# Kernel tuning notes

Hardware: AMD Instinct MI355X
Metric: run time of the kernel (lower is better)

Reference implementation:

```python
import jax, jax.numpy as jnp
import numpy as np

VAR0, VAR1 = 0.1, 0.2          # SSD variances
IOU_THRESH = 0.5
NUM_CLASSES = 21
NEGPOS_RATIO = 3
ALPHA = 1.0


def mid_to_corner(b):
    # [cx,cy,w,h] -> [xmin,ymin,xmax,ymax]
    return jnp.concatenate([b[:, :2] - b[:, 2:] / 2, b[:, :2] + b[:, 2:] / 2], axis=1)


def jaccard(box_a, box_b):
    # box_a [n,4], box_b [P,4] corner form -> IoU [n,P]
    lt = jnp.maximum(box_a[:, None, :2], box_b[None, :, :2])
    rb = jnp.minimum(box_a[:, None, 2:], box_b[None, :, 2:])
    wh = jnp.clip(rb - lt, 0.0)
    inter = wh[..., 0] * wh[..., 1]
    area_a = (box_a[:, 2] - box_a[:, 0]) * (box_a[:, 3] - box_a[:, 1])
    area_b = (box_b[:, 2] - box_b[:, 0]) * (box_b[:, 3] - box_b[:, 1])
    union = area_a[:, None] + area_b[None, :] - inter
    return inter / union


def encode_offset(matched, priors):
    # matched corner form [P,4], priors center form [P,4]
    g_cxcy = ((matched[:, :2] + matched[:, 2:]) / 2 - priors[:, :2]) / (VAR0 * priors[:, 2:])
    g_wh = jnp.log((matched[:, 2:] - matched[:, :2]) / priors[:, 2:]) / VAR1
    return jnp.concatenate([g_cxcy, g_wh], axis=1)


def match_one(gt_box, gt_cls, valid, priors_corner, priors_mid):
    # gt_box [n,4], gt_cls [n], valid [n] bool; priors [P,4]
    n = gt_box.shape[0]
    P = priors_corner.shape[0]
    ovl = jaccard(gt_box, priors_corner)                    # [n,P]
    ovl = jnp.where(valid[:, None], ovl, -1.0)              # mask padded GTs
    best_truth_idx = jnp.argmax(ovl, axis=0)                # [P]
    best_truth_ovl = jnp.max(ovl, axis=0)                   # [P]
    best_prior_idx = jnp.argmax(ovl, axis=1)                # [n]
    bpi = jnp.where(valid, best_prior_idx, P)               # OOB for padded -> dropped
    best_truth_ovl = best_truth_ovl.at[bpi].set(2.0, mode='drop')
    best_truth_idx = best_truth_idx.at[bpi].set(jnp.arange(n), mode='drop')
    matches = gt_box[best_truth_idx]                        # [P,4]
    loc = encode_offset(matches, priors_mid)                # [P,4]
    conf = gt_cls[best_truth_idx].astype(jnp.int32) + 1     # [P]
    conf = jnp.where(best_truth_ovl < IOU_THRESH, 0, conf)
    return loc, conf


def setup_inputs() -> dict:
    key = jax.random.key(0)
    k = jax.random.split(key, 8)
    B, P, C, NMAX = 64, 8732, 21, 50
    confidence = jax.random.normal(k[0], (B, P, C), dtype=jnp.float32)
    location = 0.1 * jax.random.normal(k[1], (B, P, 4), dtype=jnp.float32)
    cxcy = jax.random.uniform(k[2], (P, 2), minval=0.05, maxval=0.95)
    pwh = jax.random.uniform(k[3], (P, 2), minval=0.05, maxval=0.4)
    prior_boxes = jnp.concatenate([cxcy, pwh], axis=1).astype(jnp.float32)
    xymin = jax.random.uniform(k[4], (B, NMAX, 2), minval=0.0, maxval=0.6)
    gwh = jax.random.uniform(k[5], (B, NMAX, 2), minval=0.05, maxval=0.35)
    cls = jax.random.randint(k[6], (B, NMAX), 0, C - 1).astype(jnp.float32)
    labels = jnp.concatenate([xymin, xymin + gwh, cls[..., None]], axis=-1).astype(jnp.float32)
    obj_count = jax.random.randint(k[7], (B, 1), 1, NMAX + 1).astype(jnp.int32)
    return {"confidence": confidence, "location": location,
            "prior_boxes": prior_boxes, "labels": labels, "obj_count": obj_count}


def reference(confidence, location, prior_boxes, labels, obj_count):
    B, P, C = confidence.shape
    NMAX = labels.shape[1]
    priors_corner = mid_to_corner(prior_boxes)
    valid = jnp.arange(NMAX)[None, :] < obj_count            # [B,NMAX]
    loc_t, conf_t = jax.vmap(match_one, in_axes=(0, 0, 0, None, None))(
        labels[..., :4], labels[..., 4], valid, priors_corner, prior_boxes)
    # loc_t [B,P,4] float, conf_t [B,P] int32

    pos = conf_t > 0                                          # [B,P]
    # smooth-L1 over positive anchors (sum reduction)
    d = jnp.abs(location - loc_t)
    sl1 = jnp.where(d < 1.0, 0.5 * d * d, d - 0.5)
    loss_loc = jnp.sum(sl1 * pos[..., None].astype(sl1.dtype))

    # hard negative mining score: global-max logsumexp minus target logit
    bc = confidence.reshape(-1, C)
    x_max = jnp.max(bc)
    lse = jnp.log(jnp.sum(jnp.exp(bc - x_max), axis=1)) + x_max
    tgt_logit = jnp.take_along_axis(bc, conf_t.reshape(-1, 1), axis=1)[:, 0]
    loss_c = (lse - tgt_logit).reshape(B, P)
    loss_c = jnp.where(pos, 0.0, loss_c)
    loss_idx = jnp.argsort(-loss_c, axis=1)                   # descending sort
    idx_rank = jnp.argsort(loss_idx, axis=1)
    num_pos = jnp.sum(pos.astype(jnp.int32), axis=1, keepdims=True)   # [B,1]
    num_neg = jnp.clip(NEGPOS_RATIO * num_pos, None, P - 1)
    neg = idx_rank < num_neg                                  # [B,P]

    # standard cross entropy over selected (pos|neg) anchors, sum reduction
    logp = jax.nn.log_softmax(confidence, axis=-1)            # [B,P,C]
    nll = -jnp.take_along_axis(logp, conf_t[..., None], axis=-1)[..., 0]
    sel = jnp.logical_or(pos, neg)
    loss_conf = jnp.sum(nll * sel.astype(nll.dtype))

    N = jnp.sum(num_pos).astype(confidence.dtype)
    return (ALPHA * loss_loc / N, loss_conf / N)
```

## Files before the change

kernel.cpp:

```cpp
#include <hip/hip_runtime.h>
#include <math.h>

#define Bn 64
#define Pn 8732
#define Cn 21
#define NMAXn 50
#define PX 35
#define Wn 16

template <int C>
__device__ __forceinline__ float dppf(float x) {
    return __int_as_float(__builtin_amdgcn_update_dpp(0, __float_as_int(x), C, 0xf, 0xf, true));
}
template <int C>
__device__ __forceinline__ int dppi(int x) {
    return __builtin_amdgcn_update_dpp(0, x, C, 0xf, 0xf, true);
}
__device__ __forceinline__ float wave_max_f(float x) {
    x = fmaxf(x, dppf<0x111>(x));
    x = fmaxf(x, dppf<0x112>(x));
    x = fmaxf(x, dppf<0x114>(x));
    x = fmaxf(x, dppf<0x118>(x));
    x = fmaxf(x, dppf<0x142>(x));
    x = fmaxf(x, dppf<0x143>(x));
    return x;
}
__device__ __forceinline__ float wave_sum_f(float x) {
    x += dppf<0x111>(x); x += dppf<0x112>(x); x += dppf<0x114>(x);
    x += dppf<0x118>(x); x += dppf<0x142>(x); x += dppf<0x143>(x);
    return x;
}
__device__ __forceinline__ int wave_sum_i(int x) {
    x += dppi<0x111>(x); x += dppi<0x112>(x); x += dppi<0x114>(x);
    x += dppi<0x118>(x); x += dppi<0x142>(x); x += dppi<0x143>(x);
    return x;
}

__global__ __launch_bounds__(256) void k_bpp(const float* __restrict__ labels,
                                             const int* __restrict__ objc,
                                             const float* __restrict__ priors,
                                             int* __restrict__ match,
                                             unsigned long long* __restrict__ bpk) {
    const int b = blockIdx.y;
    const int px = blockIdx.x;
    const int tid = threadIdx.x;
    const int lane = tid & 63, wid = tid >> 6;
    const int cnt = objc[b];
    const float* lb = labels + b * NMAXn * 5;

    const int p = px * 256 + tid;
    const bool valid = p < Pn;
    const int pcl = valid ? p : (Pn - 1);
    const float4 pr = reinterpret_cast<const float4*>(priors)[pcl];
    const float px0 = pr.x - 0.5f * pr.z, py0 = pr.y - 0.5f * pr.w;
    const float px1 = pr.x + 0.5f * pr.z, py1 = pr.y + 0.5f * pr.w;
    const float parea = (px1 - px0) * (py1 - py0);

    float best = -1.0f;
    int bidx = 0;
    for (int n = 0; n < cnt; ++n) {
        const float gx0 = lb[n * 5 + 0], gy0 = lb[n * 5 + 1];
        const float gx1 = lb[n * 5 + 2], gy1 = lb[n * 5 + 3];
        const float lx = fmaxf(gx0, px0), ly = fmaxf(gy0, py0);
        const float rx = fminf(gx1, px1), ry = fminf(gy1, py1);
        const float w = fmaxf(rx - lx, 0.0f), h = fmaxf(ry - ly, 0.0f);
        const float inter = w * h;
        const float ga = (gx1 - gx0) * (gy1 - gy0);
        const float q = inter / (ga + parea - inter);
        if (q > best) { best = q; bidx = n; }
        const float qr = valid ? q : 0.0f;
        const float m = wave_max_f(qr);
        const float s_q = __int_as_float(__builtin_amdgcn_readlane(__float_as_int(m), 63));
        const unsigned long long mask = __ballot(qr == s_q);
        const int first = __ffsll(mask) - 1;
        if (lane == 0) {
            const int pw = px * 256 + (wid << 6) + first;
            const unsigned long long key =
                ((unsigned long long)__float_as_uint(s_q) << 32) |
                (unsigned long long)(65535 - pw);
            bpk[(size_t)(b * NMAXn + n) * (PX * 4) + px * 4 + wid] = key;
        }
    }
    if (valid) match[(size_t)b * Pn + p] = (bidx << 1) | (best >= 0.5f ? 1 : 0);
}

__global__ __launch_bounds__(64) void k_bpr(const int* __restrict__ objc,
                                            const unsigned long long* __restrict__ bpk,
                                            int* __restrict__ match,
                                            int* __restrict__ done) {
    __shared__ int sbp[NMAXn];
    const int b = blockIdx.x;
    const int tid = threadIdx.x;
    if (b == 0 && tid == 0) *done = 0;
    const int cnt = objc[b];
    if (tid < cnt) {
        const size_t g0 = (size_t)(b * NMAXn + tid) * (PX * 4);
        unsigned long long best = 0ull;
        for (int t = 0; t < PX * 4; ++t) {
            const unsigned long long k = bpk[g0 + t];
            best = (k > best) ? k : best;
        }
        sbp[tid] = 65535 - (int)(best & 0xFFFFull);
    }
    __syncthreads();
    if (tid < cnt) {
        const int myp = sbp[tid];
        bool win = true;
        for (int n2 = tid + 1; n2 < cnt; ++n2) win = win && (sbp[n2] != myp);
        if (win) match[(size_t)b * Pn + myp] = (tid << 1) | 1;
    }
}

__global__ __launch_bounds__(256) void k_main(const float* __restrict__ conf,
                                              const float* __restrict__ loc,
                                              const float* __restrict__ priors,
                                              const float* __restrict__ labels,
                                              const int* __restrict__ match,
                                              float* __restrict__ lc,
                                              float* __restrict__ part_loc,
                                              float* __restrict__ part_nll,
                                              int* __restrict__ part_np) {
    const int b = blockIdx.y;
    const int px = blockIdx.x;
    const int p0 = px * 256;
    const int tid = threadIdx.x;
    const int rows = min(256, Pn - p0);
    const int p = p0 + ((tid < rows) ? tid : 0);
    const size_t gi = (size_t)b * Pn + p;
    const int w = match[gi];

    const float* row = conf + gi * Cn;
    float a[Cn];
#pragma unroll
    for (int j = 0; j < Cn; ++j) a[j] = row[j];

    float my_loc = 0.0f, my_nll = 0.0f;
    int my_np = 0;
    if (tid < rows) {
        const int ti = w >> 1;
        int ct = 0;
        if (w & 1) ct = (int)labels[(b * NMAXn + ti) * 5 + 4] + 1;
        float m = a[0];
#pragma unroll
        for (int j = 1; j < Cn; ++j) m = fmaxf(m, a[j]);
        float s2 = 0.0f;
#pragma unroll
        for (int j = 0; j < Cn; ++j) s2 += __expf(a[j] - m);
        float tgt = a[0];
#pragma unroll
        for (int j = 1; j < Cn; ++j) tgt = (ct == j) ? a[j] : tgt;
        const float nll = __logf(s2) + m - tgt;
        if (ct > 0) {
            lc[gi] = 0.0f;
            my_np = 1;
            my_nll = nll;
            const float* lbp = labels + (b * NMAXn + ti) * 5;
            const float gx0 = lbp[0], gy0 = lbp[1], gx1 = lbp[2], gy1 = lbp[3];
            const float4 pr = reinterpret_cast<const float4*>(priors)[p];
            const float tx = ((gx0 + gx1) * 0.5f - pr.x) / (0.1f * pr.z);
            const float ty = ((gy0 + gy1) * 0.5f - pr.y) / (0.1f * pr.w);
            const float tw = __logf((gx1 - gx0) / pr.z) * 5.0f;
            const float th = __logf((gy1 - gy0) / pr.w) * 5.0f;
            const float4 l = reinterpret_cast<const float4*>(loc)[gi];
            float d;
            d = fabsf(l.x - tx); my_loc += (d < 1.0f) ? 0.5f * d * d : d - 0.5f;
            d = fabsf(l.y - ty); my_loc += (d < 1.0f) ? 0.5f * d * d : d - 0.5f;
            d = fabsf(l.z - tw); my_loc += (d < 1.0f) ? 0.5f * d * d : d - 0.5f;
            d = fabsf(l.w - th); my_loc += (d < 1.0f) ? 0.5f * d * d : d - 0.5f;
        } else {
            lc[gi] = nll;
        }
    }
    my_loc = wave_sum_f(my_loc);
    my_nll = wave_sum_f(my_nll);
    my_np = wave_sum_i(my_np);
    __shared__ float rl[4], rn[4];
    __shared__ int rp[4];
    const int wid = tid >> 6, lane = tid & 63;
    if (lane == 63) { rl[wid] = my_loc; rn[wid] = my_nll; rp[wid] = my_np; }
    __syncthreads();
    if (tid == 0) {
        const int g = b * PX + px;
        part_loc[g] = rl[0] + rl[1] + rl[2] + rl[3];
        part_nll[g] = rn[0] + rn[1] + rn[2] + rn[3];
        part_np[g] = rp[0] + rp[1] + rp[2] + rp[3];
    }
}

__global__ __launch_bounds__(1024) void k_neg(const float* __restrict__ lc,
                                              const float* __restrict__ part_loc,
                                              const float* __restrict__ part_nll,
                                              const int* __restrict__ part_np,
                                              float* __restrict__ negsum,
                                              int* __restrict__ done,
                                              float* __restrict__ out) {
    const int b = blockIdx.x;
    const int tid = threadIdx.x;
    const int lane = tid & 63, wid = tid >> 6;
    __shared__ int redc[2][Wn];
    __shared__ float redf[Wn], redf2[Wn];
    __shared__ int redi[Wn];
    __shared__ int np_sh, islast;

    const int NV = Pn / 4;
    const float4* src = reinterpret_cast<const float4*>(lc + (size_t)b * Pn);
    const float4 sent = make_float4(-1.0f, -1.0f, -1.0f, -1.0f);
    float4 r0 = (tid < NV) ? src[tid] : sent;
    float4 r1 = (tid + 1024 < NV) ? src[tid + 1024] : sent;
    float4 r2 = (tid + 2048 < NV) ? src[tid + 2048] : sent;

    if (tid < 64) {
        int npl = (tid < PX) ? part_np[b * PX + tid] : 0;
        npl = wave_sum_i(npl);
        if (tid == 63) np_sh = npl;
    }
    __syncthreads();
    const int k = min(3 * np_sh, Pn - 1);

    unsigned lo = 0u, hi = 0x7F800000u;
#pragma unroll 1
    for (int it = 0; it < 31; ++it) {
        const unsigned mid = lo + ((hi - lo) >> 1);
        const float fm = __uint_as_float(mid);
        int c = (r0.x >= fm) + (r0.y >= fm) + (r0.z >= fm) + (r0.w >= fm)
              + (r1.x >= fm) + (r1.y >= fm) + (r1.z >= fm) + (r1.w >= fm)
              + (r2.x >= fm) + (r2.y >= fm) + (r2.z >= fm) + (r2.w >= fm);
        c = wave_sum_i(c);
        if (lane == 63) redc[it & 1][wid] = c;
        __syncthreads();
        int tot = 0;
#pragma unroll
        for (int w = 0; w < Wn; ++w) tot += redc[it & 1][w];
        if (tot >= k) lo = mid;
        else hi = mid;
    }
    const float v = __uint_as_float(lo);

    float sm = 0.0f;
    int c = 0;
    if (r0.x > v) { sm += r0.x; ++c; }
    if (r0.y > v) { sm += r0.y; ++c; }
    if (r0.z > v) { sm += r0.z; ++c; }
    if (r0.w > v) { sm += r0.w; ++c; }
    if (r1.x > v) { sm += r1.x; ++c; }
    if (r1.y > v) { sm += r1.y; ++c; }
    if (r1.z > v) { sm += r1.z; ++c; }
    if (r1.w > v) { sm += r1.w; ++c; }
    if (r2.x > v) { sm += r2.x; ++c; }
    if (r2.y > v) { sm += r2.y; ++c; }
    if (r2.z > v) { sm += r2.z; ++c; }
    if (r2.w > v) { sm += r2.w; ++c; }
    sm = wave_sum_f(sm);
    c = wave_sum_i(c);
    if (lane == 63) { redf[wid] = sm; redi[wid] = c; }
    __syncthreads();
    if (tid == 0) {
        float st = 0.0f;
        int ct = 0;
#pragma unroll
        for (int w = 0; w < Wn; ++w) { st += redf[w]; ct += redi[w]; }
        negsum[b] = st + (float)(k - ct) * v;
        __threadfence();
        islast = (atomicAdd(done, 1) == Bn - 1) ? 1 : 0;
    }
    __syncthreads();
    if (!islast) return;
    __threadfence();

    float sl = 0.0f, sn = 0.0f;
    int np = 0;
    for (int i = tid; i < Bn * PX; i += 1024) {
        sl += part_loc[i];
        sn += part_nll[i];
        np += part_np[i];
    }
    if (tid < Bn) sn += negsum[tid];
    sl = wave_sum_f(sl);
    sn = wave_sum_f(sn);
    np = wave_sum_i(np);
    if (lane == 63) { redf[wid] = sn; redf2[wid] = sl; redi[wid] = np; }
    __syncthreads();
    if (tid == 0) {
        float tsl = 0.0f, tsn = 0.0f;
        int tnp = 0;
#pragma unroll
        for (int w = 0; w < Wn; ++w) { tsl += redf2[w]; tsn += redf[w]; tnp += redi[w]; }
        const float fN = (float)tnp;
        out[0] = tsl / fN;
        out[1] = tsn / fN;
    }
}

extern "C" void kernel_launch(void* const* d_in, const int* in_sizes, int n_in,
                              void* d_out, int out_size, void* d_ws, size_t ws_size,
                              hipStream_t stream) {
    const float* conf = (const float*)d_in[0];
    const float* loc = (const float*)d_in[1];
    const float* priors = (const float*)d_in[2];
    const float* labels = (const float*)d_in[3];
    const int* objc = (const int*)d_in[4];
    float* out = (float*)d_out;

    unsigned long long* bpk = (unsigned long long*)d_ws;
    float* part_loc = (float*)(bpk + (size_t)Bn * NMAXn * PX * 4);
    float* part_nll = part_loc + Bn * PX;
    int* part_np = (int*)(part_nll + Bn * PX);
    float* negsum = (float*)(part_np + Bn * PX);
    int* match = (int*)(negsum + Bn);
    float* lc = (float*)(match + (size_t)Bn * Pn);
    int* done = (int*)(lc + (size_t)Bn * Pn);

    dim3 g(PX, Bn);
    k_bpp<<<g, 256, 0, stream>>>(labels, objc, priors, match, bpk);
    k_bpr<<<Bn, 64, 0, stream>>>(objc, bpk, match, done);
    k_main<<<g, 256, 0, stream>>>(conf, loc, priors, labels, match, lc,
                                  part_loc, part_nll, part_np);
    k_neg<<<Bn, 1024, 0, stream>>>(lc, part_loc, part_nll, part_np, negsum, done, out);
}
```

Measured before the change: 78.65 us.

## Fuse matching, forced-match fixup and loss pass into one kernel

Merges the three kernels for per-prior matching, best-prior reduction and the per-anchor loss into one kernel. Each block now stages its confidence rows in shared memory, reduces per-GT best-prior keys with a global atomicMax, and the last block of each image computes correction terms for priors forced to a GT. Those corrections are passed to the negative-mining kernel, which zeroes the forced priors' scores. This removes two launches and the round trip of the match array through global memory. In exchange it adds a memset, atomics, a serial per-image fixup in the last block, and recomputation of IoU and loss for forced priors.

Measured after the change: 242.8 us. 3.09x slower.

```diff
diff --git a/kernel.cpp b/kernel.cpp
--- a/kernel.cpp
+++ b/kernel.cpp
@@ -17,12 +17,9 @@
     return __builtin_amdgcn_update_dpp(0, x, C, 0xf, 0xf, true);
 }
 __device__ __forceinline__ float wave_max_f(float x) {
-    x = fmaxf(x, dppf<0x111>(x));
-    x = fmaxf(x, dppf<0x112>(x));
-    x = fmaxf(x, dppf<0x114>(x));
-    x = fmaxf(x, dppf<0x118>(x));
-    x = fmaxf(x, dppf<0x142>(x));
-    x = fmaxf(x, dppf<0x143>(x));
+    x = fmaxf(x, dppf<0x111>(x)); x = fmaxf(x, dppf<0x112>(x));
+    x = fmaxf(x, dppf<0x114>(x)); x = fmaxf(x, dppf<0x118>(x));
+    x = fmaxf(x, dppf<0x142>(x)); x = fmaxf(x, dppf<0x143>(x));
     return x;
 }
 __device__ __forceinline__ float wave_sum_f(float x) {
@@ -36,26 +33,65 @@
     return x;
 }
 
-__global__ __launch_bounds__(256) void k_bpp(const float* __restrict__ labels,
+__device__ __forceinline__ float smoothl1_enc(const float4 l, const float4 pr,
+                                              float gx0, float gy0, float gx1, float gy1) {
+    const float tx = ((gx0 + gx1) * 0.5f - pr.x) / (0.1f * pr.z);
+    const float ty = ((gy0 + gy1) * 0.5f - pr.y) / (0.1f * pr.w);
+    const float tw = __logf((gx1 - gx0) / pr.z) * 5.0f;
+    const float th = __logf((gy1 - gy0) / pr.w) * 5.0f;
+    float s = 0.0f, d;
+    d = fabsf(l.x - tx); s += (d < 1.0f) ? 0.5f * d * d : d - 0.5f;
+    d = fabsf(l.y - ty); s += (d < 1.0f) ? 0.5f * d * d : d - 0.5f;
+    d = fabsf(l.z - tw); s += (d < 1.0f) ? 0.5f * d * d : d - 0.5f;
+    d = fabsf(l.w - th); s += (d < 1.0f) ? 0.5f * d * d : d - 0.5f;
+    return s;
+}
+
+__global__ __launch_bounds__(256) void k_all(const float* __restrict__ conf,
+                                             const float* __restrict__ loc,
+                                             const float* __restrict__ priors,
+                                             const float* __restrict__ labels,
                                              const int* __restrict__ objc,
-                                             const float* __restrict__ priors,
-                                             int* __restrict__ match,
-                                             unsigned long long* __restrict__ bpk) {
+                                             float* __restrict__ lc,
+                                             float* __restrict__ part_loc,
+                                             float* __restrict__ part_nll,
+                                             int* __restrict__ part_np,
+                                             unsigned long long* __restrict__ slot,
+                                             int* __restrict__ done_b,
+                                             int* __restrict__ fix_np,
+                                             float* __restrict__ fix_nll,
+                                             float* __restrict__ fix_loc,
+                                             int* __restrict__ forced_cnt,
+                                             int* __restrict__ flist) {
     const int b = blockIdx.y;
     const int px = blockIdx.x;
+    const int p0 = px * 256;
     const int tid = threadIdx.x;
     const int lane = tid & 63, wid = tid >> 6;
+    const int rows = min(256, Pn - p0);
     const int cnt = objc[b];
     const float* lb = labels + b * NMAXn * 5;
 
-    const int p = px * 256 + tid;
+    __shared__ float sconf[256 * Cn];
+    __shared__ float lab[NMAXn * 5];
+    __shared__ unsigned long long wkey[NMAXn][4];
+    __shared__ float rl[4], rn[4];
+    __shared__ int rp[4];
+    __shared__ int sbp[NMAXn];
+    __shared__ int islast_s;
+
+    const float4* src = reinterpret_cast<const float4*>(conf + ((size_t)b * Pn + p0) * Cn);
+    const int n4 = rows * Cn / 4;
+    for (int i = tid; i < n4; i += 256) reinterpret_cast<float4*>(sconf)[i] = src[i];
+    for (int i = tid; i < NMAXn * 5; i += 256) lab[i] = labels[b * NMAXn * 5 + i];
+
+    const int p = p0 + tid;
     const bool valid = p < Pn;
     const int pcl = valid ? p : (Pn - 1);
     const float4 pr = reinterpret_cast<const float4*>(priors)[pcl];
     const float px0 = pr.x - 0.5f * pr.z, py0 = pr.y - 0.5f * pr.w;
     const float px1 = pr.x + 0.5f * pr.z, py1 = pr.y + 0.5f * pr.w;
     const float parea = (px1 - px0) * (py1 - py0);
-
     float best = -1.0f;
     int bidx = 0;
     for (int n = 0; n < cnt; ++n) {
@@ -69,104 +105,46 @@
         const float q = inter / (ga + parea - inter);
         if (q > best) { best = q; bidx = n; }
         const float qr = valid ? q : 0.0f;
-        const float m = wave_max_f(qr);
-        const float s_q = __int_as_float(__builtin_amdgcn_readlane(__float_as_int(m), 63));
-        const unsigned long long mask = __ballot(qr == s_q);
-        const int first = __ffsll(mask) - 1;
+        const float mx = wave_max_f(qr);
+        const float s_q = __int_as_float(__builtin_amdgcn_readlane(__float_as_int(mx), 63));
+        const unsigned long long bmask = __ballot(qr == s_q);
         if (lane == 0) {
-            const int pw = px * 256 + (wid << 6) + first;
-            const unsigned long long key =
-                ((unsigned long long)__float_as_uint(s_q) << 32) |
-                (unsigned long long)(65535 - pw);
-            bpk[(size_t)(b * NMAXn + n) * (PX * 4) + px * 4 + wid] = key;
-        }
-    }
-    if (valid) match[(size_t)b * Pn + p] = (bidx << 1) | (best >= 0.5f ? 1 : 0);
-}
-
-__global__ __launch_bounds__(64) void k_bpr(const int* __restrict__ objc,
-                                            const unsigned long long* __restrict__ bpk,
-                                            int* __restrict__ match,
-                                            int* __restrict__ done) {
-    __shared__ int sbp[NMAXn];
-    const int b = blockIdx.x;
-    const int tid = threadIdx.x;
-    if (b == 0 && tid == 0) *done = 0;
-    const int cnt = objc[b];
+            const int first = __ffsll(bmask) - 1;
+            const int pw = p0 + (wid << 6) + first;
+            wkey[n][wid] = ((unsigned long long)__float_as_uint(s_q) << 32) |
+                           (unsigned long long)(65535 - pw);
+        }
+    }
+    __syncthreads();
+
     if (tid < cnt) {
-        const size_t g0 = (size_t)(b * NMAXn + tid) * (PX * 4);
-        unsigned long long best = 0ull;
-        for (int t = 0; t < PX * 4; ++t) {
-            const unsigned long long k = bpk[g0 + t];
-            best = (k > best) ? k : best;
-        }
-        sbp[tid] = 65535 - (int)(best & 0xFFFFull);
-    }
-    __syncthreads();
-    if (tid < cnt) {
-        const int myp = sbp[tid];
-        bool win = true;
-        for (int n2 = tid + 1; n2 < cnt; ++n2) win = win && (sbp[n2] != myp);
-        if (win) match[(size_t)b * Pn + myp] = (tid << 1) | 1;
-    }
-}
-
-__global__ __launch_bounds__(256) void k_main(const float* __restrict__ conf,
-                                              const float* __restrict__ loc,
-                                              const float* __restrict__ priors,
-                                              const float* __restrict__ labels,
-                                              const int* __restrict__ match,
-                                              float* __restrict__ lc,
-                                              float* __restrict__ part_loc,
-                                              float* __restrict__ part_nll,
-                                              int* __restrict__ part_np) {
-    const int b = blockIdx.y;
-    const int px = blockIdx.x;
-    const int p0 = px * 256;
-    const int tid = threadIdx.x;
-    const int rows = min(256, Pn - p0);
-    const int p = p0 + ((tid < rows) ? tid : 0);
-    const size_t gi = (size_t)b * Pn + p;
-    const int w = match[gi];
-
-    const float* row = conf + gi * Cn;
-    float a[Cn];
-#pragma unroll
-    for (int j = 0; j < Cn; ++j) a[j] = row[j];
+        unsigned long long kk = wkey[tid][0];
+        kk = (wkey[tid][1] > kk) ? wkey[tid][1] : kk;
+        kk = (wkey[tid][2] > kk) ? wkey[tid][2] : kk;
+        kk = (wkey[tid][3] > kk) ? wkey[tid][3] : kk;
+        atomicMax(&slot[b * NMAXn + tid], kk);
+    }
 
     float my_loc = 0.0f, my_nll = 0.0f;
     int my_np = 0;
     if (tid < rows) {
-        const int ti = w >> 1;
-        int ct = 0;
-        if (w & 1) ct = (int)labels[(b * NMAXn + ti) * 5 + 4] + 1;
-        float m = a[0];
-#pragma unroll
-        for (int j = 1; j < Cn; ++j) m = fmaxf(m, a[j]);
+        const size_t gi = (size_t)b * Pn + p;
+        const int ct = (best >= 0.5f) ? ((int)lab[bidx * 5 + 4] + 1) : 0;
+        const float* row = sconf + tid * Cn;
+        float m = row[0];
+#pragma unroll
+        for (int j = 1; j < Cn; ++j) m = fmaxf(m, row[j]);
         float s2 = 0.0f;
 #pragma unroll
-        for (int j = 0; j < Cn; ++j) s2 += __expf(a[j] - m);
-        float tgt = a[0];
-#pragma unroll
-        for (int j = 1; j < Cn; ++j) tgt = (ct == j) ? a[j] : tgt;
-        const float nll = __logf(s2) + m - tgt;
+        for (int j = 0; j < Cn; ++j) s2 += __expf(row[j] - m);
+        const float nll = __logf(s2) + m - row[ct];
         if (ct > 0) {
             lc[gi] = 0.0f;
             my_np = 1;
             my_nll = nll;
-            const float* lbp = labels + (b * NMAXn + ti) * 5;
-            const float gx0 = lbp[0], gy0 = lbp[1], gx1 = lbp[2], gy1 = lbp[3];
-            const float4 pr = reinterpret_cast<const float4*>(priors)[p];
-            const float tx = ((gx0 + gx1) * 0.5f - pr.x) / (0.1f * pr.z);
-            const float ty = ((gy0 + gy1) * 0.5f - pr.y) / (0.1f * pr.w);
-            const float tw = __logf((gx1 - gx0) / pr.z) * 5.0f;
-            const float th = __logf((gy1 - gy0) / pr.w) * 5.0f;
             const float4 l = reinterpret_cast<const float4*>(loc)[gi];
-            float d;
-            d = fabsf(l.x - tx); my_loc += (d < 1.0f) ? 0.5f * d * d : d - 0.5f;
-            d = fabsf(l.y - ty); my_loc += (d < 1.0f) ? 0.5f * d * d : d - 0.5f;
-            d = fabsf(l.z - tw); my_loc += (d < 1.0f) ? 0.5f * d * d : d - 0.5f;
-            d = fabsf(l.w - th); my_loc += (d < 1.0f) ? 0.5f * d * d : d - 0.5f;
+            my_loc = smoothl1_enc(l, pr, lab[bidx * 5 + 0], lab[bidx * 5 + 1],
+                                  lab[bidx * 5 + 2], lab[bidx * 5 + 3]);
         } else {
             lc[gi] = nll;
         }
@@ -174,9 +152,6 @@
     my_loc = wave_sum_f(my_loc);
     my_nll = wave_sum_f(my_nll);
     my_np = wave_sum_i(my_np);
-    __shared__ float rl[4], rn[4];
-    __shared__ int rp[4];
-    const int wid = tid >> 6, lane = tid & 63;
     if (lane == 63) { rl[wid] = my_loc; rn[wid] = my_nll; rp[wid] = my_np; }
     __syncthreads();
     if (tid == 0) {
@@ -185,12 +160,92 @@
         part_nll[g] = rn[0] + rn[1] + rn[2] + rn[3];
         part_np[g] = rp[0] + rp[1] + rp[2] + rp[3];
     }
+
+    __threadfence();
+    __syncthreads();
+    if (tid == 0) islast_s = (atomicAdd(&done_b[b], 1) == PX - 1) ? 1 : 0;
+    __syncthreads();
+    if (!islast_s) return;
+
+    if (tid < cnt) {
+        const unsigned long long key = slot[b * NMAXn + tid];
+        sbp[tid] = 65535 - (int)(key & 0xFFFFull);
+    }
+    __syncthreads();
+    bool win = false;
+    if (tid < cnt) {
+        const int myp = sbp[tid];
+        win = true;
+        for (int n2 = tid + 1; n2 < cnt; ++n2) win = win && (sbp[n2] != myp);
+    }
+    const unsigned long long wmask = __ballot(win);
+    float dnll = 0.0f, dloc = 0.0f;
+    int dnp = 0;
+    if (win) {
+        const int pp = sbp[tid];
+        const float4 prf = reinterpret_cast<const float4*>(priors)[pp];
+        const float qx0 = prf.x - 0.5f * prf.z, qy0 = prf.y - 0.5f * prf.w;
+        const float qx1 = prf.x + 0.5f * prf.z, qy1 = prf.y + 0.5f * prf.w;
+        const float qarea = (qx1 - qx0) * (qy1 - qy0);
+        float best2 = -1.0f;
+        int bidx2 = 0;
+        for (int n2 = 0; n2 < cnt; ++n2) {
+            const float gx0 = lab[n2 * 5 + 0], gy0 = lab[n2 * 5 + 1];
+            const float gx1 = lab[n2 * 5 + 2], gy1 = lab[n2 * 5 + 3];
+            const float lx = fmaxf(gx0, qx0), ly = fmaxf(gy0, qy0);
+            const float rx = fminf(gx1, qx1), ry = fminf(gy1, qy1);
+            const float w = fmaxf(rx - lx, 0.0f), h = fmaxf(ry - ly, 0.0f);
+            const float inter = w * h;
+            const float ga = (gx1 - gx0) * (gy1 - gy0);
+            const float q = inter / (ga + qarea - inter);
+            if (q > best2) { best2 = q; bidx2 = n2; }
+        }
+        const float* rowg = conf + ((size_t)b * Pn + pp) * Cn;
+        float m2 = rowg[0];
+#pragma unroll
+        for (int j = 1; j < Cn; ++j) m2 = fmaxf(m2, rowg[j]);
+        float ss = 0.0f;
+#pragma unroll
+        for (int j = 0; j < Cn; ++j) ss += __expf(rowg[j] - m2);
+        const float lse = __logf(ss) + m2;
+        const int ctn = (int)lab[tid * 5 + 4] + 1;
+        const float4 lv = reinterpret_cast<const float4*>(loc)[(size_t)b * Pn + pp];
+        dnll = lse - rowg[ctn];
+        dloc = smoothl1_enc(lv, prf, lab[tid * 5 + 0], lab[tid * 5 + 1],
+                            lab[tid * 5 + 2], lab[tid * 5 + 3]);
+        dnp = 1;
+        if (best2 >= 0.5f) {
+            const int cto = (int)lab[bidx2 * 5 + 4] + 1;
+            dnll -= (lse - rowg[cto]);
+            dloc -= smoothl1_enc(lv, prf, lab[bidx2 * 5 + 0], lab[bidx2 * 5 + 1],
+                                 lab[bidx2 * 5 + 2], lab[bidx2 * 5 + 3]);
+            dnp = 0;
+        }
+        const int sidx = __popcll(wmask & ((1ull << lane) - 1));
+        flist[b * NMAXn + sidx] = pp;
+    }
+    if (wid == 0) {
+        dnll = wave_sum_f(dnll);
+        dloc = wave_sum_f(dloc);
+        dnp = wave_sum_i(dnp);
+        if (lane == 63) {
+            fix_nll[b] = dnll;
+            fix_loc[b] = dloc;
+            fix_np[b] = dnp;
+            forced_cnt[b] = (int)__popcll(wmask);
+        }
+    }
 }
 
 __global__ __launch_bounds__(1024) void k_neg(const float* __restrict__ lc,
                                               const float* __restrict__ part_loc,
                                               const float* __restrict__ part_nll,
                                               const int* __restrict__ part_np,
+                                              const int* __restrict__ fix_np,
+                                              const float* __restrict__ fix_nll,
+                                              const float* __restrict__ fix_loc,
+                                              const int* __restrict__ forced_cnt,
+                                              const int* __restrict__ flist,
                                               float* __restrict__ negsum,
                                               int* __restrict__ done,
                                               float* __restrict__ out) {
@@ -209,13 +264,29 @@
     float4 r1 = (tid + 1024 < NV) ? src[tid + 1024] : sent;
     float4 r2 = (tid + 2048 < NV) ? src[tid + 2048] : sent;
 
+    const int fcnt = forced_cnt[b];
+    for (int i = 0; i < fcnt; ++i) {
+        const int pp = flist[b * NMAXn + i];
+        const int qq = pp >> 2, cc = pp & 3;
+        if (qq == tid) {
+            if (cc == 0) r0.x = 0.0f; else if (cc == 1) r0.y = 0.0f;
+            else if (cc == 2) r0.z = 0.0f; else r0.w = 0.0f;
+        } else if (qq == tid + 1024) {
+            if (cc == 0) r1.x = 0.0f; else if (cc == 1) r1.y = 0.0f;
+            else if (cc == 2) r1.z = 0.0f; else r1.w = 0.0f;
+        } else if (qq == tid + 2048) {
+            if (cc == 0) r2.x = 0.0f; else if (cc == 1) r2.y = 0.0f;
+            else if (cc == 2) r2.z = 0.0f; else r2.w = 0.0f;
+        }
+    }
+
     if (tid < 64) {
         int npl = (tid < PX) ? part_np[b * PX + tid] : 0;
         npl = wave_sum_i(npl);
         if (tid == 63) np_sh = npl;
     }
     __syncthreads();
-    const int k = min(3 * np_sh, Pn - 1);
+    const int k = min(3 * (np_sh + fix_np[b]), Pn - 1);
 
     unsigned lo = 0u, hi = 0x7F800000u;
 #pragma unroll 1
@@ -274,7 +345,11 @@
         sn += part_nll[i];
         np += part_np[i];
     }
-    if (tid < Bn) sn += negsum[tid];
+    if (tid < Bn) {
+        sn += negsum[tid] + fix_nll[tid];
+        sl += fix_loc[tid];
+        np += fix_np[tid];
+    }
     sl = wave_sum_f(sl);
     sn = wave_sum_f(sn);
     np = wave_sum_i(np);
@@ -301,19 +376,27 @@
     const int* objc = (const int*)d_in[4];
     float* out = (float*)d_out;
 
-    unsigned long long* bpk = (unsigned long long*)d_ws;
-    float* part_loc = (float*)(bpk + (size_t)Bn * NMAXn * PX * 4);
+    float* lc = (float*)d_ws;
+    unsigned long long* slot = (unsigned long long*)((char*)d_ws + (size_t)Bn * Pn * 4);
+    int* done_b = (int*)(slot + Bn * NMAXn);
+    int* done = done_b + Bn;
+    int* fix_np = done + 1;
+    float* fix_nll = (float*)(fix_np + Bn);
+    float* fix_loc = fix_nll + Bn;
+    int* forced_cnt = (int*)(fix_loc + Bn);
+    int* flist = forced_cnt + Bn;
+    float* part_loc = (float*)(flist + Bn * NMAXn);
     float* part_nll = part_loc + Bn * PX;
     int* part_np = (int*)(part_nll + Bn * PX);
     float* negsum = (float*)(part_np + Bn * PX);
-    int* match = (int*)(negsum + Bn);
-    float* lc = (float*)(match + (size_t)Bn * Pn);
-    int* done = (int*)(lc + (size_t)Bn * Pn);
+
+    hipMemsetAsync(slot, 0, Bn * NMAXn * 8 + Bn * 4 + 4, stream);
 
     dim3 g(PX, Bn);
-    k_bpp<<<g, 256, 0, stream>>>(labels, objc, priors, match, bpk);
-    k_bpr<<<Bn, 64, 0, stream>>>(objc, bpk, match, done);
-    k_main<<<g, 256, 0, stream>>>(conf, loc, priors, labels, match, lc,
-                                  part_loc, part_nll, part_np);
-    k_neg<<<Bn, 1024, 0, stream>>>(lc, part_loc, part_nll, part_np, negsum, done, out);
-}
+    k_all<<<g, 256, 0, stream>>>(conf, loc, priors, labels, objc, lc,
+                                 part_loc, part_nll, part_np, slot, done_b,
+                                 fix_np, fix_nll, fix_loc, forced_cnt, flist);
+    k_neg<<<Bn, 1024, 0, stream>>>(lc, part_loc, part_nll, part_np,
+                                   fix_np, fix_nll, fix_loc, forced_cnt, flist,
+                                   negsum, done, out);
+}
```

## Stage confidence rows in LDS with coalesced loads; shrink negative-mining blocks to 256

Applied to the files above, without the earlier changes.

k_main now copies each block's contiguous 256x21 confidence tile and the per-batch labels into shared memory with coalesced float4 loads. This replaces the strided 21-float per-thread row reads and lets the target logit be indexed directly. k_neg drops from 1024 to 256 threads per block, with each thread holding 12 float4 registers. That reduces the number of waves combined at each of the 31 bisection barriers, but gives fewer waves per block to hide latency and raises register pressure.

Result: no change. 79.76 us (+1.4%).

```diff
diff --git a/kernel.cpp b/kernel.cpp
--- a/kernel.cpp
+++ b/kernel.cpp
@@ -6,7 +6,6 @@
 #define Cn 21
 #define NMAXn 50
 #define PX 35
-#define Wn 16
 
 template <int C>
 __device__ __forceinline__ float dppf(float x) {
@@ -17,12 +16,9 @@
     return __builtin_amdgcn_update_dpp(0, x, C, 0xf, 0xf, true);
 }
 __device__ __forceinline__ float wave_max_f(float x) {
-    x = fmaxf(x, dppf<0x111>(x));
-    x = fmaxf(x, dppf<0x112>(x));
-    x = fmaxf(x, dppf<0x114>(x));
-    x = fmaxf(x, dppf<0x118>(x));
-    x = fmaxf(x, dppf<0x142>(x));
-    x = fmaxf(x, dppf<0x143>(x));
+    x = fmaxf(x, dppf<0x111>(x)); x = fmaxf(x, dppf<0x112>(x));
+    x = fmaxf(x, dppf<0x114>(x)); x = fmaxf(x, dppf<0x118>(x));
+    x = fmaxf(x, dppf<0x142>(x)); x = fmaxf(x, dppf<0x143>(x));
     return x;
 }
 __device__ __forceinline__ float wave_sum_f(float x) {
@@ -72,8 +68,8 @@
         const float m = wave_max_f(qr);
         const float s_q = __int_as_float(__builtin_amdgcn_readlane(__float_as_int(m), 63));
         const unsigned long long mask = __ballot(qr == s_q);
-        const int first = __ffsll(mask) - 1;
         if (lane == 0) {
+            const int first = __ffsll(mask) - 1;
             const int pw = px * 256 + (wid << 6) + first;
             const unsigned long long key =
                 ((unsigned long long)__float_as_uint(s_q) << 32) |
@@ -129,34 +125,34 @@
     const size_t gi = (size_t)b * Pn + p;
     const int w = match[gi];
 
-    const float* row = conf + gi * Cn;
-    float a[Cn];
-#pragma unroll
-    for (int j = 0; j < Cn; ++j) a[j] = row[j];
+    __shared__ float sconf[256 * Cn];
+    __shared__ float lab[NMAXn * 5];
+    const float4* src = reinterpret_cast<const float4*>(conf + ((size_t)b * Pn + p0) * Cn);
+    const int n4 = rows * Cn / 4;
+    for (int i = tid; i < n4; i += 256) reinterpret_cast<float4*>(sconf)[i] = src[i];
+    for (int i = tid; i < NMAXn * 5; i += 256) lab[i] = labels[b * NMAXn * 5 + i];
+    __syncthreads();
 
     float my_loc = 0.0f, my_nll = 0.0f;
     int my_np = 0;
     if (tid < rows) {
         const int ti = w >> 1;
-        int ct = 0;
-        if (w & 1) ct = (int)labels[(b * NMAXn + ti) * 5 + 4] + 1;
-        float m = a[0];
-#pragma unroll
-        for (int j = 1; j < Cn; ++j) m = fmaxf(m, a[j]);
+        const int ct = (w & 1) ? ((int)lab[ti * 5 + 4] + 1) : 0;
+        const float* row = sconf + tid * Cn;
+        float m = row[0];
+#pragma unroll
+        for (int j = 1; j < Cn; ++j) m = fmaxf(m, row[j]);
         float s2 = 0.0f;
 #pragma unroll
-        for (int j = 0; j < Cn; ++j) s2 += __expf(a[j] - m);
-        float tgt = a[0];
-#pragma unroll
-        for (int j = 1; j < Cn; ++j) tgt = (ct == j) ? a[j] : tgt;
-        const float nll = __logf(s2) + m - tgt;
+        for (int j = 0; j < Cn; ++j) s2 += __expf(row[j] - m);
+        const float nll = __logf(s2) + m - row[ct];
         if (ct > 0) {
             lc[gi] = 0.0f;
             my_np = 1;
             my_nll = nll;
-            const float* lbp = labels + (b * NMAXn + ti) * 5;
-            const float gx0 = lbp[0], gy0 = lbp[1], gx1 = lbp[2], gy1 = lbp[3];
             const float4 pr = reinterpret_cast<const float4*>(priors)[p];
+            const float gx0 = lab[ti * 5 + 0], gy0 = lab[ti * 5 + 1];
+            const float gx1 = lab[ti * 5 + 2], gy1 = lab[ti * 5 + 3];
             const float tx = ((gx0 + gx1) * 0.5f - pr.x) / (0.1f * pr.z);
             const float ty = ((gy0 + gy1) * 0.5f - pr.y) / (0.1f * pr.w);
             const float tw = __logf((gx1 - gx0) / pr.z) * 5.0f;
@@ -187,27 +183,30 @@
     }
 }
 
-__global__ __launch_bounds__(1024) void k_neg(const float* __restrict__ lc,
-                                              const float* __restrict__ part_loc,
-                                              const float* __restrict__ part_nll,
-                                              const int* __restrict__ part_np,
-                                              float* __restrict__ negsum,
-                                              int* __restrict__ done,
-                                              float* __restrict__ out) {
+__global__ __launch_bounds__(256) void k_neg(const float* __restrict__ lc,
+                                             const float* __restrict__ part_loc,
+                                             const float* __restrict__ part_nll,
+                                             const int* __restrict__ part_np,
+                                             float* __restrict__ negsum,
+                                             int* __restrict__ done,
+                                             float* __restrict__ out) {
     const int b = blockIdx.x;
     const int tid = threadIdx.x;
     const int lane = tid & 63, wid = tid >> 6;
-    __shared__ int redc[2][Wn];
-    __shared__ float redf[Wn], redf2[Wn];
-    __shared__ int redi[Wn];
+    __shared__ int redc[2][4];
+    __shared__ float redf[4], redf2[4];
+    __shared__ int redi[4];
     __shared__ int np_sh, islast;
 
     const int NV = Pn / 4;
     const float4* src = reinterpret_cast<const float4*>(lc + (size_t)b * Pn);
     const float4 sent = make_float4(-1.0f, -1.0f, -1.0f, -1.0f);
-    float4 r0 = (tid < NV) ? src[tid] : sent;
-    float4 r1 = (tid + 1024 < NV) ? src[tid + 1024] : sent;
-    float4 r2 = (tid + 2048 < NV) ? src[tid + 2048] : sent;
+    float4 rr[12];
+#pragma unroll
+    for (int j = 0; j < 12; ++j) {
+        const int i = tid + 256 * j;
+        rr[j] = (i < NV) ? src[i] : sent;
+    }
 
     if (tid < 64) {
         int npl = (tid < PX) ? part_np[b * PX + tid] : 0;
@@ -222,15 +221,15 @@
     for (int it = 0; it < 31; ++it) {
         const unsigned mid = lo + ((hi - lo) >> 1);
         const float fm = __uint_as_float(mid);
-        int c = (r0.x >= fm) + (r0.y >= fm) + (r0.z >= fm) + (r0.w >= fm)
-              + (r1.x >= fm) + (r1.y >= fm) + (r1.z >= fm) + (r1.w >= fm)
-              + (r2.x >= fm) + (r2.y >= fm) + (r2.z >= fm) + (r2.w >= fm);
+        int c = 0;
+#pragma unroll
+        for (int j = 0; j < 12; ++j)
+            c += (rr[j].x >= fm) + (rr[j].y >= fm) + (rr[j].z >= fm) + (rr[j].w >= fm);
         c = wave_sum_i(c);
         if (lane == 63) redc[it & 1][wid] = c;
         __syncthreads();
-        int tot = 0;
-#pragma unroll
-        for (int w = 0; w < Wn; ++w) tot += redc[it & 1][w];
+        const int tot = redc[it & 1][0] + redc[it & 1][1]
+                      + redc[it & 1][2] + redc[it & 1][3];
         if (tot >= k) lo = mid;
         else hi = mid;
     }
@@ -238,27 +237,20 @@
 
     float sm = 0.0f;
     int c = 0;
-    if (r0.x > v) { sm += r0.x; ++c; }
-    if (r0.y > v) { sm += r0.y; ++c; }
-    if (r0.z > v) { sm += r0.z; ++c; }
-    if (r0.w > v) { sm += r0.w; ++c; }
-    if (r1.x > v) { sm += r1.x; ++c; }
-    if (r1.y > v) { sm += r1.y; ++c; }
-    if (r1.z > v) { sm += r1.z; ++c; }
-    if (r1.w > v) { sm += r1.w; ++c; }
-    if (r2.x > v) { sm += r2.x; ++c; }
-    if (r2.y > v) { sm += r2.y; ++c; }
-    if (r2.z > v) { sm += r2.z; ++c; }
-    if (r2.w > v) { sm += r2.w; ++c; }
+#pragma unroll
+    for (int j = 0; j < 12; ++j) {
+        if (rr[j].x > v) { sm += rr[j].x; ++c; }
+        if (rr[j].y > v) { sm += rr[j].y; ++c; }
+        if (rr[j].z > v) { sm += rr[j].z; ++c; }
+        if (rr[j].w > v) { sm += rr[j].w; ++c; }
+    }
     sm = wave_sum_f(sm);
     c = wave_sum_i(c);
     if (lane == 63) { redf[wid] = sm; redi[wid] = c; }
     __syncthreads();
     if (tid == 0) {
-        float st = 0.0f;
-        int ct = 0;
-#pragma unroll
-        for (int w = 0; w < Wn; ++w) { st += redf[w]; ct += redi[w]; }
+        const float st = redf[0] + redf[1] + redf[2] + redf[3];
+        const int ct = redi[0] + redi[1] + redi[2] + redi[3];
         negsum[b] = st + (float)(k - ct) * v;
         __threadfence();
         islast = (atomicAdd(done, 1) == Bn - 1) ? 1 : 0;
@@ -269,7 +261,7 @@
 
     float sl = 0.0f, sn = 0.0f;
     int np = 0;
-    for (int i = tid; i < Bn * PX; i += 1024) {
+    for (int i = tid; i < Bn * PX; i += 256) {
         sl += part_loc[i];
         sn += part_nll[i];
         np += part_np[i];
@@ -281,13 +273,9 @@
     if (lane == 63) { redf[wid] = sn; redf2[wid] = sl; redi[wid] = np; }
     __syncthreads();
     if (tid == 0) {
-        float tsl = 0.0f, tsn = 0.0f;
-        int tnp = 0;
-#pragma unroll
-        for (int w = 0; w < Wn; ++w) { tsl += redf2[w]; tsn += redf[w]; tnp += redi[w]; }
-        const float fN = (float)tnp;
-        out[0] = tsl / fN;
-        out[1] = tsn / fN;
+        const float fN = (float)(redi[0] + redi[1] + redi[2] + redi[3]);
+        out[0] = (redf2[0] + redf2[1] + redf2[2] + redf2[3]) / fN;
+        out[1] = (redf[0] + redf[1] + redf[2] + redf[3]) / fN;
     }
 }
 
@@ -315,5 +303,5 @@
     k_bpr<<<Bn, 64, 0, stream>>>(objc, bpk, match, done);
     k_main<<<g, 256, 0, stream>>>(conf, loc, priors, labels, match, lc,
                                   part_loc, part_nll, part_np);
-    k_neg<<<Bn, 1024, 0, stream>>>(lc, part_loc, part_nll, part_np, negsum, done, out);
-}
+    k_neg<<<Bn, 256, 0, stream>>>(lc, part_loc, part_nll, part_np, negsum, done, out);
+}
```
